# Kernel optimization log

Measured on AMD Instinct MI355X. Metric: run time of the kernel, lower is better.

The kernel has to match this reference:

```python
import jax, jax.numpy as jnp
import numpy as np


def setup_inputs() -> dict:
    key = jax.random.key(0)
    T, B, I, H = 1024, 32, 512, 512
    k1, k2, k3 = jax.random.split(key, 3)
    scale = 1.0 / np.sqrt(H)  # torch LSTM default init range
    return {
        "x": jax.random.normal(k1, (T, B, I), dtype=jnp.float32),
        "h0": jnp.zeros((1, B, H), dtype=jnp.float32),
        "c0": jnp.zeros((1, B, H), dtype=jnp.float32),
        "Wx": jax.random.normal(k2, (4 * H, I), dtype=jnp.float32) * scale,
        "Wh": jax.random.normal(k3, (4 * H, H), dtype=jnp.float32) * scale,
        "b": jnp.zeros((4 * H,), dtype=jnp.float32),
    }


def reference(x, h0, c0, Wx, Wh, b):
    """RNNLayer.forward (training path, res_link=False, single-layer LSTM).

    x:  [T, B, I] time-major input
    h0, c0: [1, B, H] initial state (num_layers = 1)
    Wx: [4H, I], Wh: [4H, H], b: [4H] with torch gate order (i, f, g, o)
    Returns (output [T,B,H], h_T [1,B,H], c_T [1,B,H], all_hidden_state [T,B,H])
    """
    H = h0.shape[-1]

    def step(carry, x_t):
        h, c = carry  # [B, H] each
        gates = x_t @ Wx.T + h @ Wh.T + b  # [B, 4H]
        i, f, g, o = jnp.split(gates, 4, axis=-1)
        c = jax.nn.sigmoid(f) * c + jax.nn.sigmoid(i) * jnp.tanh(g)
        h = jax.nn.sigmoid(o) * jnp.tanh(c)
        return (h, c), h

    (h_T, c_T), hs = jax.lax.scan(step, (h0[0], c0[0]), x)
    output = hs  # [T, B, H]
    # hidden_state_list: per-step h concatenated over time -> [T*num_layers, B, H]
    all_hidden_state = hs
    return output, h_T[None], c_T[None], all_hidden_state
```

## Files before the change

### kernel.cpp

```cpp
#include <hip/hip_runtime.h>
#include <hip/hip_bf16.h>


typedef __attribute__((ext_vector_type(8))) short short8;
typedef __attribute__((ext_vector_type(4))) float f32x4;
typedef __attribute__((ext_vector_type(4))) unsigned u32x4;

#define T_TOT 1024
#define T_CHUNK 128
#define NCHUNK 8
#define BB 32
#define HH 512
#define G4 2048
#define NBLK 16
#define SENT32 0x7F807F80u

__device__ __forceinline__ unsigned short f2bf(float x) {
  union { float f; unsigned u; } v; v.f = x;
  unsigned r = v.u + 0x7FFFu + ((v.u >> 16) & 1u);
  return (unsigned short)(r >> 16);
}

__device__ __forceinline__ float bf2f(unsigned short h) {
  union { unsigned u; float f; } v; v.u = ((unsigned)h) << 16;
  return v.f;
}

__device__ __forceinline__ f32x4 mfma16(short8 a, short8 b, f32x4 c) {
  return __builtin_amdgcn_mfma_f32_16x16x32_bf16(a, b, c, 0, 0, 0);
}

__device__ __forceinline__ unsigned chk4(u32x4 a) {
  return (a.x != SENT32) & (a.y != SENT32) & (a.z != SENT32) & (a.w != SENT32);
}

__global__ void fill_sentinel(uint4* __restrict__ p, int n16) {
  int i = blockIdx.x * blockDim.x + threadIdx.x;
  if (i >= n16) return;
  uint4 v; v.x = SENT32; v.y = SENT32; v.z = SENT32; v.w = SENT32;
  p[i] = v;
}

__global__ void cvt_bf16_kernel(const float* __restrict__ src,
                                unsigned short* __restrict__ dst, int n8) {
  int i = blockIdx.x * blockDim.x + threadIdx.x;
  if (i >= n8) return;
  const float4* s4 = (const float4*)src;
  float4 a = s4[2 * i], b = s4[2 * i + 1];
  short8 o;
  o[0] = (short)f2bf(a.x); o[1] = (short)f2bf(a.y);
  o[2] = (short)f2bf(a.z); o[3] = (short)f2bf(a.w);
  o[4] = (short)f2bf(b.x); o[5] = (short)f2bf(b.y);
  o[6] = (short)f2bf(b.z); o[7] = (short)f2bf(b.w);
  *(short8*)(dst + 8 * i) = o;
}

__global__ __launch_bounds__(256) void expand_out(
    const unsigned short* __restrict__ hseq, float* __restrict__ out,
    long long ahO) {
  long long i = (long long)blockIdx.x * blockDim.x + threadIdx.x;
  long long e = i * 8;
  const short8 v = *(const short8*)(hseq + BB * HH + e);
  float4 lo, hi;
  lo.x = bf2f((unsigned short)v[0]); lo.y = bf2f((unsigned short)v[1]);
  lo.z = bf2f((unsigned short)v[2]); lo.w = bf2f((unsigned short)v[3]);
  hi.x = bf2f((unsigned short)v[4]); hi.y = bf2f((unsigned short)v[5]);
  hi.z = bf2f((unsigned short)v[6]); hi.w = bf2f((unsigned short)v[7]);
  *(float4*)(out + e) = lo;
  *(float4*)(out + e + 4) = hi;
  *(float4*)(out + ahO + e) = lo;
  *(float4*)(out + ahO + e + 4) = hi;
}

__global__ void final_state(const unsigned short* __restrict__ hseq,
                            const float* __restrict__ cbuf,
                            float* __restrict__ out, long long hTO,
                            long long cTO) {
  int i = blockIdx.x * blockDim.x + threadIdx.x;
  if (i >= BB * HH) return;
  out[hTO + i] = bf2f(hseq[(size_t)T_TOT * BB * HH + i]);
  out[cTO + i] = cbuf[i];
}

__global__ __launch_bounds__(256) void gemm_gx(
    const unsigned short* __restrict__ A,
    const unsigned short* __restrict__ Bw,
    float* __restrict__ C)
{
  __shared__ short As[128 * 64];
  __shared__ short Bs[128 * 64];
  const int tid = threadIdx.x;
  const int lane = tid & 63, wave = tid >> 6;
  const int wm = wave >> 1, wn = wave & 1;
  const int m0 = blockIdx.y * 128, n0 = blockIdx.x * 128;
  const int r = lane & 15, kg = lane >> 4;

  const f32x4 vzero = {0.f, 0.f, 0.f, 0.f};
  f32x4 acc[4][4];
#pragma unroll
  for (int i = 0; i < 4; ++i)
#pragma unroll
    for (int j = 0; j < 4; ++j) acc[i][j] = vzero;

  for (int kt = 0; kt < 8; ++kt) {
    const int k0 = kt * 64;
#pragma unroll
    for (int j = 0; j < 4; ++j) {
      int e = j * 2048 + tid * 8;
      int row = e >> 6, col = e & 63;
      *(short8*)(As + e) = *(const short8*)(A + (m0 + row) * 512 + k0 + col);
      *(short8*)(Bs + e) = *(const short8*)(Bw + (n0 + row) * 512 + k0 + col);
    }
    __syncthreads();
#pragma unroll
    for (int ks = 0; ks < 2; ++ks) {
      short8 af[4], bfr[4];
#pragma unroll
      for (int mi = 0; mi < 4; ++mi)
        af[mi] = *(const short8*)(As + (wm * 64 + mi * 16 + r) * 64 + ks * 32 + kg * 8);
#pragma unroll
      for (int ni = 0; ni < 4; ++ni)
        bfr[ni] = *(const short8*)(Bs + (wn * 64 + ni * 16 + r) * 64 + ks * 32 + kg * 8);
#pragma unroll
      for (int mi = 0; mi < 4; ++mi)
#pragma unroll
        for (int ni = 0; ni < 4; ++ni)
          acc[mi][ni] = mfma16(af[mi], bfr[ni], acc[mi][ni]);
    }
    __syncthreads();
  }
  const int cc = lane & 15, rr4 = (lane >> 4) * 4;
#pragma unroll
  for (int mi = 0; mi < 4; ++mi) {
#pragma unroll
    for (int ni = 0; ni < 4; ++ni) {
      int gm = m0 + wm * 64 + mi * 16 + rr4;
      int gn = n0 + wn * 64 + ni * 16 + cc;
#pragma unroll
      for (int j = 0; j < 4; ++j) C[(gm + j) * 2048 + gn] = acc[mi][ni][j];
    }
  }
}

__global__ __launch_bounds__(512, 1) void lstm_seq(
    const float* __restrict__ gx,
    const unsigned short* __restrict__ Whb,
    const float* __restrict__ bias,
    const float* __restrict__ c0,
    unsigned short* __restrict__ hseq,
    float* __restrict__ cbuf,
    int* __restrict__ claim,
    int chunkIdx)
{
  const int tid = threadIdx.x;

  __shared__ int sg;
  if (tid == 0) {
    unsigned xcc;
    asm volatile("s_getreg_b32 %0, hwreg(HW_REG_XCC_ID)" : "=s"(xcc));
    xcc &= 7u;
    int tk = -1;
    if (xcc == 0) {
      tk = atomicAdd(&claim[chunkIdx], 1);
    } else {
      int cnt = 0;
      for (int i = 0; i < 64; ++i) {
        cnt = __hip_atomic_load(&claim[chunkIdx], __ATOMIC_RELAXED,
                                __HIP_MEMORY_SCOPE_AGENT);
        if (cnt >= NBLK) break;
        __builtin_amdgcn_s_sleep(127);
      }
      if (cnt < NBLK)
        tk = atomicAdd(&claim[chunkIdx], 1);
    }
    sg = tk;
  }
  __syncthreads();
  const int g = sg;
  if (g < 0 || g >= NBLK) return;

  const int t0 = chunkIdx * T_CHUNK;
  const int lane = tid & 63, wave = tid >> 6;
  const int mt = wave >> 2, nt = wave & 3;
  const int r = lane & 15, kg = lane >> 4;

  short8 bfrag[2][16];
#pragma unroll
  for (int ct = 0; ct < 2; ++ct) {
    const int urow = nt * HH + g * 32 + ct * 16 + r;
#pragma unroll
    for (int s = 0; s < 16; ++s)
      bfrag[ct][s] = *(const short8*)((const short*)Whb + urow * HH + s * 32 + kg * 8);
  }
#pragma unroll
  for (int ct = 0; ct < 2; ++ct)
#pragma unroll
    for (int s = 0; s < 16; ++s)
      asm volatile("" : "+v"(bfrag[ct][s]));

  const int b = tid >> 4, u2 = (tid & 15) * 2;
  const int unit0 = g * 32 + u2;
  const float bi0 = bias[0 * HH + unit0], bi1 = bias[0 * HH + unit0 + 1];
  const float bf0 = bias[1 * HH + unit0], bf1 = bias[1 * HH + unit0 + 1];
  const float bg0 = bias[2 * HH + unit0], bg1 = bias[2 * HH + unit0 + 1];
  const float bo0 = bias[3 * HH + unit0], bo1 = bias[3 * HH + unit0 + 1];
  float cst0, cst1;
  if (t0 == 0) { cst0 = c0[b * HH + unit0]; cst1 = c0[b * HH + unit0 + 1]; }
  else         { cst0 = cbuf[b * HH + unit0]; cst1 = cbuf[b * HH + unit0 + 1]; }

  __shared__ unsigned short hs[BB * HH];
  __shared__ float gbuf[4][BB][33];

  const int srow = tid >> 4;
  const int sb = (tid & 15) * 16;
  const int sswz = (srow & 7) << 4;

  float2 xi, xf, xg, xo;
  {
    const float* gxp = gx + (long long)b * G4 + unit0;
    xi = *(const float2*)(gxp + 0 * HH);
    xf = *(const float2*)(gxp + 1 * HH);
    xg = *(const float2*)(gxp + 2 * HH);
    xo = *(const float2*)(gxp + 3 * HH);
  }

  for (int tt = 0; tt < T_CHUNK; ++tt) {
    const int t = t0 + tt;

    const char* hqb = (const char*)hseq + (size_t)t * (BB * HH * 2) +
                      (size_t)srow * 1024 + sb;
    u32x4 p0, p1, p2, p3;
    {
      unsigned guard = 0;
      while (true) {
        asm volatile(
            "global_load_dwordx4 %0, %4, off sc1\n\t"
            "global_load_dwordx4 %1, %4, off offset:256 sc1\n\t"
            "global_load_dwordx4 %2, %4, off offset:512 sc1\n\t"
            "global_load_dwordx4 %3, %4, off offset:768 sc1\n\t"
            "s_waitcnt vmcnt(0)"
            : "=&v"(p0), "=&v"(p1), "=&v"(p2), "=&v"(p3)
            : "v"(hqb)
            : "memory");
        if (chk4(p0) & chk4(p1) & chk4(p2) & chk4(p3)) break;
        if (++guard > 8192) break;
      }
    }
    {
      const int base = srow * 1024 + sb;
      *(u32x4*)((char*)hs + ((base + 0) ^ sswz)) = p0;
      *(u32x4*)((char*)hs + ((base + 256) ^ sswz)) = p1;
      *(u32x4*)((char*)hs + ((base + 512) ^ sswz)) = p2;
      *(u32x4*)((char*)hs + ((base + 768) ^ sswz)) = p3;
    }

    float2 nxi, nxf, nxg, nxo;
    {
      const int tn = (tt + 1 < T_CHUNK) ? tt + 1 : tt;
      const float* gxp = gx + (long long)tn * BB * G4 + b * G4 + unit0;
      nxi = *(const float2*)(gxp + 0 * HH);
      nxf = *(const float2*)(gxp + 1 * HH);
      nxg = *(const float2*)(gxp + 2 * HH);
      nxo = *(const float2*)(gxp + 3 * HH);
    }
    __syncthreads();

    f32x4 aE0 = {0, 0, 0, 0}, aO0 = {0, 0, 0, 0};
    f32x4 aE1 = {0, 0, 0, 0}, aO1 = {0, 0, 0, 0};
    const int abase = (mt * 16 + r) * 1024;
    const int aswz = (r & 7) << 4;
#pragma unroll
    for (int s = 0; s < 16; s += 2) {
      short8 a0f = *(const short8*)((const char*)hs + ((abase + s * 64 + kg * 16) ^ aswz));
      short8 a1f = *(const short8*)((const char*)hs + ((abase + (s + 1) * 64 + kg * 16) ^ aswz));
      aE0 = mfma16(a0f, bfrag[0][s], aE0);
      aE1 = mfma16(a0f, bfrag[1][s], aE1);
      aO0 = mfma16(a1f, bfrag[0][s + 1], aO0);
      aO1 = mfma16(a1f, bfrag[1][s + 1], aO1);
    }
    const f32x4 acc0 = aE0 + aO0, acc1 = aE1 + aO1;
#pragma unroll
    for (int j = 0; j < 4; ++j) {
      gbuf[nt][mt * 16 + kg * 4 + j][r] = acc0[j];
      gbuf[nt][mt * 16 + kg * 4 + j][16 + r] = acc1[j];
    }
    __syncthreads();

    float gi0 = gbuf[0][b][u2] + xi.x + bi0, gi1 = gbuf[0][b][u2 + 1] + xi.y + bi1;
    float gf0_ = gbuf[1][b][u2] + xf.x + bf0, gf1_ = gbuf[1][b][u2 + 1] + xf.y + bf1;
    float gg0 = gbuf[2][b][u2] + xg.x + bg0, gg1 = gbuf[2][b][u2 + 1] + xg.y + bg1;
    float go0 = gbuf[3][b][u2] + xo.x + bo0, go1 = gbuf[3][b][u2 + 1] + xo.y + bo1;
    float si0 = 1.f / (1.f + __expf(-gi0)), si1 = 1.f / (1.f + __expf(-gi1));
    float sf0 = 1.f / (1.f + __expf(-gf0_)), sf1 = 1.f / (1.f + __expf(-gf1_));
    float so0 = 1.f / (1.f + __expf(-go0)), so1 = 1.f / (1.f + __expf(-go1));
    float tg0 = 2.f / (1.f + __expf(-2.f * gg0)) - 1.f;
    float tg1 = 2.f / (1.f + __expf(-2.f * gg1)) - 1.f;
    cst0 = sf0 * cst0 + si0 * tg0;
    cst1 = sf1 * cst1 + si1 * tg1;
    float tc0 = 2.f / (1.f + __expf(-2.f * cst0)) - 1.f;
    float tc1 = 2.f / (1.f + __expf(-2.f * cst1)) - 1.f;
    float hn0 = so0 * tc0, hn1 = so1 * tc1;

    unsigned w32 = (unsigned)f2bf(hn0) | ((unsigned)f2bf(hn1) << 16);
    char* pa = (char*)hseq + (size_t)(t + 1) * (BB * HH * 2) +
               (size_t)(b * HH + unit0) * 2;
    asm volatile("global_store_dword %0, %1, off sc1"
                 :: "v"(pa), "v"(w32) : "memory");

    xi = nxi; xf = nxf; xg = nxg; xo = nxo;

    if (tt == T_CHUNK - 1) {
      cbuf[b * HH + unit0] = cst0;
      cbuf[b * HH + unit0 + 1] = cst1;
    }
  }
}

extern "C" void kernel_launch(void* const* d_in, const int* in_sizes, int n_in,
                              void* d_out, int out_size, void* d_ws, size_t ws_size,
                              hipStream_t stream) {
  const float* x  = (const float*)d_in[0];
  const float* h0 = (const float*)d_in[1];
  const float* c0 = (const float*)d_in[2];
  const float* Wx = (const float*)d_in[3];
  const float* Wh = (const float*)d_in[4];
  const float* b  = (const float*)d_in[5];
  float* out = (float*)d_out;
  char* ws = (char*)d_ws;

  float* gx            = (float*)ws;
  unsigned short* xb   = (unsigned short*)(ws + 33554432);
  unsigned short* Wxb  = (unsigned short*)(ws + 67108864);
  unsigned short* Whb  = (unsigned short*)(ws + 69206016);
  unsigned short* hseq = (unsigned short*)(ws + 71303168);
  float* cbuf          = (float*)(ws + 104923136);
  int* claim           = (int*)(ws + 104988672);

  const long long hTO = (long long)T_TOT * BB * HH;
  const long long cTO = hTO + BB * HH;
  const long long ahO = cTO + BB * HH;

  (void)hipMemsetAsync(claim, 0, NCHUNK * sizeof(int), stream);

  const int n16 = (1025 * BB * HH * 2) / 16;
  fill_sentinel<<<(n16 + 255) / 256, 256, 0, stream>>>((uint4*)hseq, n16);

  cvt_bf16_kernel<<<8192, 256, 0, stream>>>(x, xb, 16777216 / 8);
  cvt_bf16_kernel<<<512, 256, 0, stream>>>(Wx, Wxb, 1048576 / 8);
  cvt_bf16_kernel<<<512, 256, 0, stream>>>(Wh, Whb, 1048576 / 8);
  cvt_bf16_kernel<<<8, 256, 0, stream>>>(h0, hseq, 16384 / 8);

  for (int ch = 0; ch < NCHUNK; ++ch) {
    gemm_gx<<<dim3(16, 32), 256, 0, stream>>>(xb + (size_t)ch * 4096 * 512, Wxb, gx);
    lstm_seq<<<256, 512, 0, stream>>>(gx, Whb, b, c0, hseq, cbuf, claim, ch);
  }

  expand_out<<<8192, 256, 0, stream>>>(hseq, out, ahO);
  final_state<<<64, 256, 0, stream>>>(hseq, cbuf, out, hTO, cTO);
}
```

Before: 2.646 ms.

## Prefetch next-step hidden state early and keep own slice locally in LDS

Measured after the change: 4.866 ms. +83.9%, slower.

```diff
diff --git a/kernel.cpp b/kernel.cpp
--- a/kernel.cpp
+++ b/kernel.cpp
@@ -214,6 +214,11 @@
   const int srow = tid >> 4;
   const int sb = (tid & 15) * 16;
   const int sswz = (srow & 7) << 4;
+  const unsigned own0 = (((sb >> 6) + 0) == g) ? 1u : 0u;
+  const unsigned own1 = (((sb >> 6) + 4) == g) ? 1u : 0u;
+  const unsigned own2 = (((sb >> 6) + 8) == g) ? 1u : 0u;
+  const unsigned own3 = (((sb >> 6) + 12) == g) ? 1u : 0u;
+  const int ownLds = (b * 1024 + (g * 64 + u2 * 2)) ^ ((b & 7) << 4);
 
   float2 xi, xf, xg, xo;
   {
@@ -224,34 +229,73 @@
     xo = *(const float2*)(gxp + 3 * HH);
   }
 
+  u32x4 pA0, pA1, pA2, pA3;
+  {
+    const char* hqb = (const char*)hseq + (size_t)t0 * (BB * HH * 2) +
+                      (size_t)srow * 1024 + sb;
+    asm volatile(
+        "global_load_dwordx4 %0, %4, off sc1\n\t"
+        "global_load_dwordx4 %1, %4, off offset:256 sc1\n\t"
+        "global_load_dwordx4 %2, %4, off offset:512 sc1\n\t"
+        "global_load_dwordx4 %3, %4, off offset:768 sc1"
+        : "=&v"(pA0), "=&v"(pA1), "=&v"(pA2), "=&v"(pA3)
+        : "v"(hqb)
+        : "memory");
+  }
+
   for (int tt = 0; tt < T_CHUNK; ++tt) {
     const int t = t0 + tt;
-
     const char* hqb = (const char*)hseq + (size_t)t * (BB * HH * 2) +
                       (size_t)srow * 1024 + sb;
-    u32x4 p0, p1, p2, p3;
-    {
+
+    if (tt == 0) {
+      asm volatile("s_waitcnt vmcnt(0)"
+                   : "+v"(pA0), "+v"(pA1), "+v"(pA2), "+v"(pA3)
+                   :: "memory");
+      __builtin_amdgcn_sched_barrier(0);
       unsigned guard = 0;
-      while (true) {
+      while (!(chk4(pA0) & chk4(pA1) & chk4(pA2) & chk4(pA3))) {
+        if (++guard > 8192) break;
         asm volatile(
             "global_load_dwordx4 %0, %4, off sc1\n\t"
             "global_load_dwordx4 %1, %4, off offset:256 sc1\n\t"
             "global_load_dwordx4 %2, %4, off offset:512 sc1\n\t"
             "global_load_dwordx4 %3, %4, off offset:768 sc1\n\t"
             "s_waitcnt vmcnt(0)"
-            : "=&v"(p0), "=&v"(p1), "=&v"(p2), "=&v"(p3)
+            : "=&v"(pA0), "=&v"(pA1), "=&v"(pA2), "=&v"(pA3)
             : "v"(hqb)
             : "memory");
-        if (chk4(p0) & chk4(p1) & chk4(p2) & chk4(p3)) break;
+      }
+    } else {
+      asm volatile("s_waitcnt vmcnt(1)"
+                   : "+v"(pA0), "+v"(pA1), "+v"(pA2), "+v"(pA3)
+                   :: "memory");
+      __builtin_amdgcn_sched_barrier(0);
+      unsigned ok = (own0 | chk4(pA0)) & (own1 | chk4(pA1)) &
+                    (own2 | chk4(pA2)) & (own3 | chk4(pA3));
+      unsigned guard = 0;
+      while (!ok) {
         if (++guard > 8192) break;
+        asm volatile(
+            "global_load_dwordx4 %0, %4, off sc1\n\t"
+            "global_load_dwordx4 %1, %4, off offset:256 sc1\n\t"
+            "global_load_dwordx4 %2, %4, off offset:512 sc1\n\t"
+            "global_load_dwordx4 %3, %4, off offset:768 sc1\n\t"
+            "s_waitcnt vmcnt(0)"
+            : "=&v"(pA0), "=&v"(pA1), "=&v"(pA2), "=&v"(pA3)
+            : "v"(hqb)
+            : "memory");
+        ok = (own0 | chk4(pA0)) & (own1 | chk4(pA1)) &
+             (own2 | chk4(pA2)) & (own3 | chk4(pA3));
       }
     }
+
     {
       const int base = srow * 1024 + sb;
-      *(u32x4*)((char*)hs + ((base + 0) ^ sswz)) = p0;
-      *(u32x4*)((char*)hs + ((base + 256) ^ sswz)) = p1;
-      *(u32x4*)((char*)hs + ((base + 512) ^ sswz)) = p2;
-      *(u32x4*)((char*)hs + ((base + 768) ^ sswz)) = p3;
+      if (tt == 0 || !own0) *(u32x4*)((char*)hs + ((base + 0) ^ sswz)) = pA0;
+      if (tt == 0 || !own1) *(u32x4*)((char*)hs + ((base + 256) ^ sswz)) = pA1;
+      if (tt == 0 || !own2) *(u32x4*)((char*)hs + ((base + 512) ^ sswz)) = pA2;
+      if (tt == 0 || !own3) *(u32x4*)((char*)hs + ((base + 768) ^ sswz)) = pA3;
     }
 
     float2 nxi, nxf, nxg, nxo;
@@ -301,11 +345,27 @@
     float tc1 = 2.f / (1.f + __expf(-2.f * cst1)) - 1.f;
     float hn0 = so0 * tc0, hn1 = so1 * tc1;
 
-    unsigned w32 = (unsigned)f2bf(hn0) | ((unsigned)f2bf(hn1) << 16);
-    char* pa = (char*)hseq + (size_t)(t + 1) * (BB * HH * 2) +
-               (size_t)(b * HH + unit0) * 2;
-    asm volatile("global_store_dword %0, %1, off sc1"
-                 :: "v"(pa), "v"(w32) : "memory");
+    const unsigned w32 = (unsigned)f2bf(hn0) | ((unsigned)f2bf(hn1) << 16);
+
+    {
+      const char* hqn = (const char*)hseq + (size_t)(t + 1) * (BB * HH * 2) +
+                        (size_t)srow * 1024 + sb;
+      asm volatile(
+          "global_load_dwordx4 %0, %4, off sc1\n\t"
+          "global_load_dwordx4 %1, %4, off offset:256 sc1\n\t"
+          "global_load_dwordx4 %2, %4, off offset:512 sc1\n\t"
+          "global_load_dwordx4 %3, %4, off offset:768 sc1"
+          : "=&v"(pA0), "=&v"(pA1), "=&v"(pA2), "=&v"(pA3)
+          : "v"(hqn)
+          : "memory");
+    }
+    {
+      char* pa = (char*)hseq + (size_t)(t + 1) * (BB * HH * 2) +
+                 (size_t)(b * HH + unit0) * 2;
+      asm volatile("global_store_dword %0, %1, off sc1"
+                   :: "v"(pa), "v"(w32) : "memory");
+    }
+    *(unsigned*)((char*)hs + ownLds) = w32;
 
     xi = nxi; xf = nxf; xg = nxg; xo = nxo;
 
@@ -314,6 +374,7 @@
       cbuf[b * HH + unit0 + 1] = cst1;
     }
   }
+  asm volatile("s_waitcnt vmcnt(0)" ::: "memory");
 }
 
 extern "C" void kernel_launch(void* const* d_in, const int* in_sizes, int n_in,
```

## Permute global h layout so waves load MFMA fragments directly, drop LDS staging

Applied to the files above, without the earlier changes.

Result: slower. 10.02 ms (+278.6%).

```diff
diff --git a/kernel.cpp b/kernel.cpp
--- a/kernel.cpp
+++ b/kernel.cpp
@@ -32,6 +32,10 @@
 
 __device__ __forceinline__ unsigned chk4(u32x4 a) {
   return (a.x != SENT32) & (a.y != SENT32) & (a.z != SENT32) & (a.w != SENT32);
+}
+
+__device__ __forceinline__ short8 as_s8(u32x4 a) {
+  union { u32x4 u; short8 s; } v; v.u = a; return v.s;
 }
 
 __global__ void fill_sentinel(uint4* __restrict__ p, int n16) {
@@ -55,12 +59,34 @@
   *(short8*)(dst + 8 * i) = o;
 }
 
+__global__ void cvt_h0_perm(const float* __restrict__ src,
+                            unsigned short* __restrict__ dst, int nch) {
+  int i = blockIdx.x * blockDim.x + threadIdx.x;
+  if (i >= nch) return;
+  int row = i >> 6, c = i & 63;
+  int p = (c & 3) * 16 + (c >> 2);
+  const float4* s4 = (const float4*)(src + i * 8);
+  float4 a = s4[0], b = s4[1];
+  short8 o;
+  o[0] = (short)f2bf(a.x); o[1] = (short)f2bf(a.y);
+  o[2] = (short)f2bf(a.z); o[3] = (short)f2bf(a.w);
+  o[4] = (short)f2bf(b.x); o[5] = (short)f2bf(b.y);
+  o[6] = (short)f2bf(b.z); o[7] = (short)f2bf(b.w);
+  *(short8*)(dst + row * 512 + p * 8) = o;
+}
+
 __global__ __launch_bounds__(256) void expand_out(
     const unsigned short* __restrict__ hseq, float* __restrict__ out,
     long long ahO) {
   long long i = (long long)blockIdx.x * blockDim.x + threadIdx.x;
   long long e = i * 8;
-  const short8 v = *(const short8*)(hseq + BB * HH + e);
+  int t = (int)(e >> 14);
+  int rem = (int)(e & 16383);
+  int b = rem >> 9, u = rem & 511;
+  int c = u >> 3;
+  int p = (c & 3) * 16 + (c >> 2);
+  const short8 v =
+      *(const short8*)(hseq + (size_t)(t + 1) * 16384 + b * 512 + p * 8);
   float4 lo, hi;
   lo.x = bf2f((unsigned short)v[0]); lo.y = bf2f((unsigned short)v[1]);
   lo.z = bf2f((unsigned short)v[2]); lo.w = bf2f((unsigned short)v[3]);
@@ -78,7 +104,9 @@
                             long long cTO) {
   int i = blockIdx.x * blockDim.x + threadIdx.x;
   if (i >= BB * HH) return;
-  out[hTO + i] = bf2f(hseq[(size_t)T_TOT * BB * HH + i]);
+  int b = i >> 9, u = i & 511, c = u >> 3, j = u & 7;
+  int p = (c & 3) * 16 + (c >> 2);
+  out[hTO + i] = bf2f(hseq[(size_t)T_TOT * 16384 + b * 512 + p * 8 + j]);
   out[cTO + i] = cbuf[i];
 }
 
@@ -208,12 +236,10 @@
   if (t0 == 0) { cst0 = c0[b * HH + unit0]; cst1 = c0[b * HH + unit0 + 1]; }
   else         { cst0 = cbuf[b * HH + unit0]; cst1 = cbuf[b * HH + unit0 + 1]; }
 
-  __shared__ unsigned short hs[BB * HH];
-  __shared__ float gbuf[4][BB][33];
-
-  const int srow = tid >> 4;
-  const int sb = (tid & 15) * 16;
-  const int sswz = (srow & 7) << 4;
+  __shared__ float gbuf[2][4][BB][33];
+
+  const size_t fragoff = (size_t)((mt * 16 + r) * 1024 + kg * 256);
+  const size_t puboff = (size_t)(b * 1024 + ((u2 >> 3) * 16 + g) * 16 + (u2 & 7) * 2);
 
   float2 xi, xf, xg, xo;
   {
@@ -226,32 +252,44 @@
 
   for (int tt = 0; tt < T_CHUNK; ++tt) {
     const int t = t0 + tt;
-
-    const char* hqb = (const char*)hseq + (size_t)t * (BB * HH * 2) +
-                      (size_t)srow * 1024 + sb;
-    u32x4 p0, p1, p2, p3;
+    const int par = tt & 1;
+
+    const char* hqb = (const char*)hseq + (size_t)t * 32768 + fragoff;
+    u32x4 F0, F1, F2, F3, F4, F5, F6, F7, F8, F9, F10, F11, F12, F13, F14, F15;
     {
       unsigned guard = 0;
       while (true) {
         asm volatile(
-            "global_load_dwordx4 %0, %4, off sc1\n\t"
-            "global_load_dwordx4 %1, %4, off offset:256 sc1\n\t"
-            "global_load_dwordx4 %2, %4, off offset:512 sc1\n\t"
-            "global_load_dwordx4 %3, %4, off offset:768 sc1\n\t"
+            "global_load_dwordx4 %0, %16, off sc1\n\t"
+            "global_load_dwordx4 %1, %16, off offset:16 sc1\n\t"
+            "global_load_dwordx4 %2, %16, off offset:32 sc1\n\t"
+            "global_load_dwordx4 %3, %16, off offset:48 sc1\n\t"
+            "global_load_dwordx4 %4, %16, off offset:64 sc1\n\t"
+            "global_load_dwordx4 %5, %16, off offset:80 sc1\n\t"
+            "global_load_dwordx4 %6, %16, off offset:96 sc1\n\t"
+            "global_load_dwordx4 %7, %16, off offset:112 sc1\n\t"
+            "global_load_dwordx4 %8, %16, off offset:128 sc1\n\t"
+            "global_load_dwordx4 %9, %16, off offset:144 sc1\n\t"
+            "global_load_dwordx4 %10, %16, off offset:160 sc1\n\t"
+            "global_load_dwordx4 %11, %16, off offset:176 sc1\n\t"
+            "global_load_dwordx4 %12, %16, off offset:192 sc1\n\t"
+            "global_load_dwordx4 %13, %16, off offset:208 sc1\n\t"
+            "global_load_dwordx4 %14, %16, off offset:224 sc1\n\t"
+            "global_load_dwordx4 %15, %16, off offset:240 sc1\n\t"
             "s_waitcnt vmcnt(0)"
-            : "=&v"(p0), "=&v"(p1), "=&v"(p2), "=&v"(p3)
+            : "=&v"(F0), "=&v"(F1), "=&v"(F2), "=&v"(F3),
+              "=&v"(F4), "=&v"(F5), "=&v"(F6), "=&v"(F7),
+              "=&v"(F8), "=&v"(F9), "=&v"(F10), "=&v"(F11),
+              "=&v"(F12), "=&v"(F13), "=&v"(F14), "=&v"(F15)
             : "v"(hqb)
             : "memory");
-        if (chk4(p0) & chk4(p1) & chk4(p2) & chk4(p3)) break;
+        unsigned ok = chk4(F0) & chk4(F1) & chk4(F2) & chk4(F3) &
+                      chk4(F4) & chk4(F5) & chk4(F6) & chk4(F7) &
+                      chk4(F8) & chk4(F9) & chk4(F10) & chk4(F11) &
+                      chk4(F12) & chk4(F13) & chk4(F14) & chk4(F15);
+        if (ok) break;
         if (++guard > 8192) break;
       }
-    }
-    {
-      const int base = srow * 1024 + sb;
-      *(u32x4*)((char*)hs + ((base + 0) ^ sswz)) = p0;
-      *(u32x4*)((char*)hs + ((base + 256) ^ sswz)) = p1;
-      *(u32x4*)((char*)hs + ((base + 512) ^ sswz)) = p2;
-      *(u32x4*)((char*)hs + ((base + 768) ^ sswz)) = p3;
     }
 
     float2 nxi, nxf, nxg, nxo;
@@ -263,33 +301,31 @@
       nxg = *(const float2*)(gxp + 2 * HH);
       nxo = *(const float2*)(gxp + 3 * HH);
     }
-    __syncthreads();
 
     f32x4 aE0 = {0, 0, 0, 0}, aO0 = {0, 0, 0, 0};
     f32x4 aE1 = {0, 0, 0, 0}, aO1 = {0, 0, 0, 0};
-    const int abase = (mt * 16 + r) * 1024;
-    const int aswz = (r & 7) << 4;
-#pragma unroll
-    for (int s = 0; s < 16; s += 2) {
-      short8 a0f = *(const short8*)((const char*)hs + ((abase + s * 64 + kg * 16) ^ aswz));
-      short8 a1f = *(const short8*)((const char*)hs + ((abase + (s + 1) * 64 + kg * 16) ^ aswz));
-      aE0 = mfma16(a0f, bfrag[0][s], aE0);
-      aE1 = mfma16(a0f, bfrag[1][s], aE1);
-      aO0 = mfma16(a1f, bfrag[0][s + 1], aO0);
-      aO1 = mfma16(a1f, bfrag[1][s + 1], aO1);
-    }
+#define PSTEP(S0, S1, FA, FB)                        \
+    aE0 = mfma16(as_s8(FA), bfrag[0][S0], aE0);      \
+    aE1 = mfma16(as_s8(FA), bfrag[1][S0], aE1);      \
+    aO0 = mfma16(as_s8(FB), bfrag[0][S1], aO0);      \
+    aO1 = mfma16(as_s8(FB), bfrag[1][S1], aO1);
+    PSTEP(0, 1, F0, F1)   PSTEP(2, 3, F2, F3)
+    PSTEP(4, 5, F4, F5)   PSTEP(6, 7, F6, F7)
+    PSTEP(8, 9, F8, F9)   PSTEP(10, 11, F10, F11)
+    PSTEP(12, 13, F12, F13) PSTEP(14, 15, F14, F15)
+#undef PSTEP
     const f32x4 acc0 = aE0 + aO0, acc1 = aE1 + aO1;
 #pragma unroll
     for (int j = 0; j < 4; ++j) {
-      gbuf[nt][mt * 16 + kg * 4 + j][r] = acc0[j];
-      gbuf[nt][mt * 16 + kg * 4 + j][16 + r] = acc1[j];
+      gbuf[par][nt][mt * 16 + kg * 4 + j][r] = acc0[j];
+      gbuf[par][nt][mt * 16 + kg * 4 + j][16 + r] = acc1[j];
     }
     __syncthreads();
 
-    float gi0 = gbuf[0][b][u2] + xi.x + bi0, gi1 = gbuf[0][b][u2 + 1] + xi.y + bi1;
-    float gf0_ = gbuf[1][b][u2] + xf.x + bf0, gf1_ = gbuf[1][b][u2 + 1] + xf.y + bf1;
-    float gg0 = gbuf[2][b][u2] + xg.x + bg0, gg1 = gbuf[2][b][u2 + 1] + xg.y + bg1;
-    float go0 = gbuf[3][b][u2] + xo.x + bo0, go1 = gbuf[3][b][u2 + 1] + xo.y + bo1;
+    float gi0 = gbuf[par][0][b][u2] + xi.x + bi0, gi1 = gbuf[par][0][b][u2 + 1] + xi.y + bi1;
+    float gf0_ = gbuf[par][1][b][u2] + xf.x + bf0, gf1_ = gbuf[par][1][b][u2 + 1] + xf.y + bf1;
+    float gg0 = gbuf[par][2][b][u2] + xg.x + bg0, gg1 = gbuf[par][2][b][u2 + 1] + xg.y + bg1;
+    float go0 = gbuf[par][3][b][u2] + xo.x + bo0, go1 = gbuf[par][3][b][u2 + 1] + xo.y + bo1;
     float si0 = 1.f / (1.f + __expf(-gi0)), si1 = 1.f / (1.f + __expf(-gi1));
     float sf0 = 1.f / (1.f + __expf(-gf0_)), sf1 = 1.f / (1.f + __expf(-gf1_));
     float so0 = 1.f / (1.f + __expf(-go0)), so1 = 1.f / (1.f + __expf(-go1));
@@ -302,8 +338,7 @@
     float hn0 = so0 * tc0, hn1 = so1 * tc1;
 
     unsigned w32 = (unsigned)f2bf(hn0) | ((unsigned)f2bf(hn1) << 16);
-    char* pa = (char*)hseq + (size_t)(t + 1) * (BB * HH * 2) +
-               (size_t)(b * HH + unit0) * 2;
+    char* pa = (char*)hseq + (size_t)(t + 1) * 32768 + puboff;
     asm volatile("global_store_dword %0, %1, off sc1"
                  :: "v"(pa), "v"(w32) : "memory");
 
@@ -314,6 +349,7 @@
       cbuf[b * HH + unit0 + 1] = cst1;
     }
   }
+  asm volatile("s_waitcnt vmcnt(0)" ::: "memory");
 }
 
 extern "C" void kernel_launch(void* const* d_in, const int* in_sizes, int n_in,
@@ -348,7 +384,7 @@
   cvt_bf16_kernel<<<8192, 256, 0, stream>>>(x, xb, 16777216 / 8);
   cvt_bf16_kernel<<<512, 256, 0, stream>>>(Wx, Wxb, 1048576 / 8);
   cvt_bf16_kernel<<<512, 256, 0, stream>>>(Wh, Whb, 1048576 / 8);
-  cvt_bf16_kernel<<<8, 256, 0, stream>>>(h0, hseq, 16384 / 8);
+  cvt_h0_perm<<<8, 256, 0, stream>>>(h0, hseq, 2048);
 
   for (int ch = 0; ch < NCHUNK; ++ch) {
     gemm_gx<<<dim3(16, 32), 256, 0, stream>>>(xb + (size_t)ch * 4096 * 512, Wxb, gx);
```

## Overlap next-chunk input GEMM with LSTM recurrence using idle blocks

Applied to the files above, without the earlier changes.

Result: slower. 3.736 ms (+41.2%).

```diff
diff --git a/kernel.cpp b/kernel.cpp
--- a/kernel.cpp
+++ b/kernel.cpp
@@ -85,7 +85,7 @@
 __global__ __launch_bounds__(256) void gemm_gx(
     const unsigned short* __restrict__ A,
     const unsigned short* __restrict__ Bw,
-    float* __restrict__ C)
+    unsigned short* __restrict__ C)
 {
   __shared__ short As[128 * 64];
   __shared__ short Bs[128 * 64];
@@ -137,24 +137,34 @@
       int gm = m0 + wm * 64 + mi * 16 + rr4;
       int gn = n0 + wn * 64 + ni * 16 + cc;
 #pragma unroll
-      for (int j = 0; j < 4; ++j) C[(gm + j) * 2048 + gn] = acc[mi][ni][j];
+      for (int j = 0; j < 4; ++j)
+        C[(size_t)(gm + j) * 2048 + gn] = f2bf(acc[mi][ni][j]);
     }
   }
 }
 
 __global__ __launch_bounds__(512, 1) void lstm_seq(
-    const float* __restrict__ gx,
+    const unsigned short* __restrict__ gxc,
+    unsigned short* __restrict__ gxn,
+    const unsigned short* __restrict__ xbn,
+    const unsigned short* __restrict__ Wxb,
     const unsigned short* __restrict__ Whb,
     const float* __restrict__ bias,
     const float* __restrict__ c0,
     unsigned short* __restrict__ hseq,
     float* __restrict__ cbuf,
     int* __restrict__ claim,
+    int* __restrict__ tiles,
     int chunkIdx)
 {
   const int tid = threadIdx.x;
 
-  __shared__ int sg;
+  __shared__ unsigned short hs[BB * HH];
+  __shared__ float gbuf[4][BB][33];
+  __shared__ short As[128 * 64];
+  __shared__ short Bs[128 * 64];
+  __shared__ int sg, sgt;
+
   if (tid == 0) {
     unsigned xcc;
     asm volatile("s_getreg_b32 %0, hwreg(HW_REG_XCC_ID)" : "=s"(xcc));
@@ -177,12 +187,70 @@
   }
   __syncthreads();
   const int g = sg;
-  if (g < 0 || g >= NBLK) return;
+  const int lane = tid & 63, wave = tid >> 6;
+  const int r = lane & 15, kg = lane >> 4;
+
+  if (g < 0 || g >= NBLK) {
+    if (chunkIdx >= NCHUNK - 1) return;
+    const int wm = wave >> 2, wn = wave & 3;
+    while (true) {
+      __syncthreads();
+      if (tid == 0) sgt = atomicAdd(&tiles[chunkIdx], 1);
+      __syncthreads();
+      const int tk = sgt;
+      if (tk >= 512) break;
+      const int m0 = (tk >> 4) * 128, n0 = (tk & 15) * 128;
+      const f32x4 vzero = {0.f, 0.f, 0.f, 0.f};
+      f32x4 acc[4][2];
+#pragma unroll
+      for (int mi = 0; mi < 4; ++mi)
+#pragma unroll
+        for (int ni = 0; ni < 2; ++ni) acc[mi][ni] = vzero;
+      for (int kt = 0; kt < 8; ++kt) {
+        const int k0 = kt * 64;
+#pragma unroll
+        for (int j = 0; j < 2; ++j) {
+          int e = j * 4096 + tid * 8;
+          int row = e >> 6, col = e & 63;
+          *(short8*)(As + e) = *(const short8*)(xbn + (m0 + row) * 512 + k0 + col);
+          *(short8*)(Bs + e) = *(const short8*)(Wxb + (n0 + row) * 512 + k0 + col);
+        }
+        __syncthreads();
+#pragma unroll
+        for (int ks = 0; ks < 2; ++ks) {
+          short8 af[4], bfr[2];
+#pragma unroll
+          for (int mi = 0; mi < 4; ++mi)
+            af[mi] = *(const short8*)(As + (wm * 64 + mi * 16 + r) * 64 + ks * 32 + kg * 8);
+#pragma unroll
+          for (int ni = 0; ni < 2; ++ni)
+            bfr[ni] = *(const short8*)(Bs + (wn * 32 + ni * 16 + r) * 64 + ks * 32 + kg * 8);
+#pragma unroll
+          for (int mi = 0; mi < 4; ++mi)
+#pragma unroll
+            for (int ni = 0; ni < 2; ++ni)
+              acc[mi][ni] = mfma16(af[mi], bfr[ni], acc[mi][ni]);
+        }
+        __syncthreads();
+      }
+      const int cc = lane & 15, rr4 = (lane >> 4) * 4;
+#pragma unroll
+      for (int mi = 0; mi < 4; ++mi) {
+#pragma unroll
+        for (int ni = 0; ni < 2; ++ni) {
+          int gm = m0 + wm * 64 + mi * 16 + rr4;
+          int gn = n0 + wn * 32 + ni * 16 + cc;
+#pragma unroll
+          for (int j = 0; j < 4; ++j)
+            gxn[(size_t)(gm + j) * 2048 + gn] = f2bf(acc[mi][ni][j]);
+        }
+      }
+    }
+    return;
+  }
 
   const int t0 = chunkIdx * T_CHUNK;
-  const int lane = tid & 63, wave = tid >> 6;
   const int mt = wave >> 2, nt = wave & 3;
-  const int r = lane & 15, kg = lane >> 4;
 
   short8 bfrag[2][16];
 #pragma unroll
@@ -208,20 +276,21 @@
   if (t0 == 0) { cst0 = c0[b * HH + unit0]; cst1 = c0[b * HH + unit0 + 1]; }
   else         { cst0 = cbuf[b * HH + unit0]; cst1 = cbuf[b * HH + unit0 + 1]; }
 
-  __shared__ unsigned short hs[BB * HH];
-  __shared__ float gbuf[4][BB][33];
-
   const int srow = tid >> 4;
   const int sb = (tid & 15) * 16;
   const int sswz = (srow & 7) << 4;
 
   float2 xi, xf, xg, xo;
   {
-    const float* gxp = gx + (long long)b * G4 + unit0;
-    xi = *(const float2*)(gxp + 0 * HH);
-    xf = *(const float2*)(gxp + 1 * HH);
-    xg = *(const float2*)(gxp + 2 * HH);
-    xo = *(const float2*)(gxp + 3 * HH);
+    const unsigned short* gxp = gxc + (size_t)b * G4 + unit0;
+    unsigned wi_ = *(const unsigned*)(gxp + 0 * HH);
+    unsigned wf_ = *(const unsigned*)(gxp + 1 * HH);
+    unsigned wg_ = *(const unsigned*)(gxp + 2 * HH);
+    unsigned wo_ = *(const unsigned*)(gxp + 3 * HH);
+    xi.x = bf2f((unsigned short)wi_); xi.y = bf2f((unsigned short)(wi_ >> 16));
+    xf.x = bf2f((unsigned short)wf_); xf.y = bf2f((unsigned short)(wf_ >> 16));
+    xg.x = bf2f((unsigned short)wg_); xg.y = bf2f((unsigned short)(wg_ >> 16));
+    xo.x = bf2f((unsigned short)wo_); xo.y = bf2f((unsigned short)(wo_ >> 16));
   }
 
   for (int tt = 0; tt < T_CHUNK; ++tt) {
@@ -257,11 +326,15 @@
     float2 nxi, nxf, nxg, nxo;
     {
       const int tn = (tt + 1 < T_CHUNK) ? tt + 1 : tt;
-      const float* gxp = gx + (long long)tn * BB * G4 + b * G4 + unit0;
-      nxi = *(const float2*)(gxp + 0 * HH);
-      nxf = *(const float2*)(gxp + 1 * HH);
-      nxg = *(const float2*)(gxp + 2 * HH);
-      nxo = *(const float2*)(gxp + 3 * HH);
+      const unsigned short* gxp = gxc + (size_t)tn * BB * G4 + b * G4 + unit0;
+      unsigned wi_ = *(const unsigned*)(gxp + 0 * HH);
+      unsigned wf_ = *(const unsigned*)(gxp + 1 * HH);
+      unsigned wg_ = *(const unsigned*)(gxp + 2 * HH);
+      unsigned wo_ = *(const unsigned*)(gxp + 3 * HH);
+      nxi.x = bf2f((unsigned short)wi_); nxi.y = bf2f((unsigned short)(wi_ >> 16));
+      nxf.x = bf2f((unsigned short)wf_); nxf.y = bf2f((unsigned short)(wf_ >> 16));
+      nxg.x = bf2f((unsigned short)wg_); nxg.y = bf2f((unsigned short)(wg_ >> 16));
+      nxo.x = bf2f((unsigned short)wo_); nxo.y = bf2f((unsigned short)(wo_ >> 16));
     }
     __syncthreads();
 
@@ -314,6 +387,7 @@
       cbuf[b * HH + unit0 + 1] = cst1;
     }
   }
+  asm volatile("s_waitcnt vmcnt(0)" ::: "memory");
 }
 
 extern "C" void kernel_launch(void* const* d_in, const int* in_sizes, int n_in,
@@ -328,19 +402,21 @@
   float* out = (float*)d_out;
   char* ws = (char*)d_ws;
 
-  float* gx            = (float*)ws;
+  unsigned short* gxA  = (unsigned short*)ws;
+  unsigned short* gxB  = (unsigned short*)(ws + 16777216);
   unsigned short* xb   = (unsigned short*)(ws + 33554432);
   unsigned short* Wxb  = (unsigned short*)(ws + 67108864);
   unsigned short* Whb  = (unsigned short*)(ws + 69206016);
   unsigned short* hseq = (unsigned short*)(ws + 71303168);
-  float* cbuf          = (float*)(ws + 104923136);
-  int* claim           = (int*)(ws + 104988672);
+  float* cbuf          = (float*)(ws + 104890368);
+  int* claim           = (int*)(ws + 104955904);
+  int* tiles           = (int*)(ws + 104955968);
 
   const long long hTO = (long long)T_TOT * BB * HH;
   const long long cTO = hTO + BB * HH;
   const long long ahO = cTO + BB * HH;
 
-  (void)hipMemsetAsync(claim, 0, NCHUNK * sizeof(int), stream);
+  (void)hipMemsetAsync(claim, 0, 128, stream);
 
   const int n16 = (1025 * BB * HH * 2) / 16;
   fill_sentinel<<<(n16 + 255) / 256, 256, 0, stream>>>((uint4*)hseq, n16);
@@ -350,9 +426,15 @@
   cvt_bf16_kernel<<<512, 256, 0, stream>>>(Wh, Whb, 1048576 / 8);
   cvt_bf16_kernel<<<8, 256, 0, stream>>>(h0, hseq, 16384 / 8);
 
+  gemm_gx<<<dim3(16, 32), 256, 0, stream>>>(xb, Wxb, gxA);
+
   for (int ch = 0; ch < NCHUNK; ++ch) {
-    gemm_gx<<<dim3(16, 32), 256, 0, stream>>>(xb + (size_t)ch * 4096 * 512, Wxb, gx);
-    lstm_seq<<<256, 512, 0, stream>>>(gx, Whb, b, c0, hseq, cbuf, claim, ch);
+    const unsigned short* gxc = (ch & 1) ? gxB : gxA;
+    unsigned short* gxn       = (ch & 1) ? gxA : gxB;
+    const int chn = (ch + 1 < NCHUNK) ? ch + 1 : 0;
+    const unsigned short* xbn = xb + (size_t)chn * 4096 * 512;
+    lstm_seq<<<256, 512, 0, stream>>>(gxc, gxn, xbn, Wxb, Whb, b, c0, hseq,
+                                      cbuf, claim, tiles, ch);
   }
 
   expand_out<<<8192, 256, 0, stream>>>(hseq, out, ahO);
```
